# Performance work log

Measured on AMD Instinct MI355X. Metric: run time of the kernel, lower is better.

## Reference

```python
import jax, jax.numpy as jnp
import numpy as np

NUM_EMBEDDINGS = 1024
EMBEDDING_DIM = 256


def setup_inputs() -> dict:
    key = jax.random.key(0)
    k1, k2 = jax.random.split(key)
    x = jax.random.normal(k1, (64, EMBEDDING_DIM, 32, 32), dtype=jnp.float32)
    # torch.nn.init.uniform_ default is U[0,1)
    embeddings = jax.random.uniform(k2, (EMBEDDING_DIM, NUM_EMBEDDINGS), dtype=jnp.float32)
    return {"x": x, "embeddings": embeddings}


def reference(x, embeddings):
    # x: [B, C, H, W] with C == embedding_dim; embeddings: [D, K]
    B, C, H, W = x.shape
    x_perm = jnp.transpose(x, (0, 2, 3, 1))           # [B, H, W, D]
    flat = x_perm.reshape(-1, C)                      # [N, D]
    sim = flat @ embeddings                           # [N, K] GEMM
    dists = (jnp.sum(flat * flat, axis=1, keepdims=True)
             + jnp.sum(embeddings * embeddings, axis=0)
             - 2.0 * sim)                             # [N, K]
    indices = jnp.argmin(dists, axis=1)               # [N]
    # one-hot @ embeddings.T is just a row gather of embeddings.T
    quantized = embeddings.T[indices]                 # [N, D]
    quantized = quantized.reshape(x_perm.shape)       # [B, H, W, D]
    # straight-through estimator
    q_ste = x_perm + jax.lax.stop_gradient(quantized - x_perm)
    q_ste = jnp.transpose(q_ste, (0, 3, 1, 2))        # [B, C, H, W]
    quantized = jnp.transpose(quantized, (0, 3, 1, 2))
    return q_ste, quantized, indices
```

## Files before the change

### kernel.cpp

```cpp
#include <hip/hip_runtime.h>

typedef unsigned short u16;
typedef unsigned int   u32;

#define DCH  256
#define KCB  1024
#define HW   1024
#define NPOS 65536
#define MARGIN 0.12f

#define ESQ_WS   0
#define IDX_WS   4096
#define FCNT_WS  266240
#define FLIST_WS 266304
#define ESQD_WS  528448ull
#define XH_WS    1048576ull
#define EH_WS    34603008ull

using f32x4 = __attribute__((ext_vector_type(4))) float;
using f16x8 = __attribute__((ext_vector_type(8))) _Float16;

__device__ __forceinline__ u16 f2h(float x) {
    _Float16 h = (_Float16)x;
    return *reinterpret_cast<u16*>(&h);
}
__device__ __forceinline__ u32 umin2(u32 a, u32 b) { return a < b ? a : b; }
__device__ __forceinline__ u32 umax2(u32 a, u32 b) { return a > b ? a : b; }

__device__ __forceinline__ void gl_lds16(const void* g, void* l) {
    __builtin_amdgcn_global_load_lds(
        (const __attribute__((address_space(1))) void*)g,
        (__attribute__((address_space(3))) void*)l, 16, 0, 0);
}

__device__ __forceinline__ void transpose_slice(const float* __restrict__ src,
                                                u16* __restrict__ dst,
                                                int b, int pc, int cc, int tid) {
    __shared__ float Xs[32][260];
    const int p0 = pc * 256;
    const int c0 = cc * 32;
    const size_t nbase = (size_t)b * 1024 + p0;
#pragma unroll
    for (int r = 0; r < 8; ++r) {
        int id4 = tid + 256 * r;
        int c = id4 >> 6;
        int q = id4 & 63;
        float4 v = *reinterpret_cast<const float4*>(
            src + (size_t)b * 262144 + (size_t)(c0 + c) * 1024 + p0 + q * 4);
        *reinterpret_cast<float4*>(&Xs[c][q * 4]) = v;
    }
    __syncthreads();
    const int p = tid;
#pragma unroll
    for (int dg = 0; dg < 4; ++dg) {
        u32 w0, w1, w2, w3;
        {
            float f0 = Xs[dg * 8 + 0][p], f1 = Xs[dg * 8 + 1][p];
            float f2 = Xs[dg * 8 + 2][p], f3 = Xs[dg * 8 + 3][p];
            float f4 = Xs[dg * 8 + 4][p], f5 = Xs[dg * 8 + 5][p];
            float f6 = Xs[dg * 8 + 6][p], f7 = Xs[dg * 8 + 7][p];
            w0 = (u32)f2h(f0) | ((u32)f2h(f1) << 16);
            w1 = (u32)f2h(f2) | ((u32)f2h(f3) << 16);
            w2 = (u32)f2h(f4) | ((u32)f2h(f5) << 16);
            w3 = (u32)f2h(f6) | ((u32)f2h(f7) << 16);
        }
        uint4 ov = {w0, w1, w2, w3};
        *reinterpret_cast<uint4*>(dst + (nbase + p) * 256 + c0 + dg * 8) = ov;
    }
}

__global__ __launch_bounds__(256) void prep_all(const float* __restrict__ X,
                                                const float* __restrict__ E,
                                                u16* __restrict__ Xh,
                                                u16* __restrict__ Eh,
                                                float* __restrict__ esq,
                                                double* __restrict__ esqd,
                                                int* __restrict__ fcnt) {
    const int tid = threadIdx.x;
    const int bid = blockIdx.x;
    if (bid < 2048) {
        transpose_slice(X, Xh, bid >> 5, (bid >> 3) & 3, bid & 7, tid);
    } else if (bid < 2080) {
        int b2 = bid - 2048;
        transpose_slice(E, Eh, 0, (b2 >> 3) & 3, b2 & 7, tid);
    } else {
        if (bid == 2080 && tid == 0) *fcnt = 0;
        int k = (bid - 2080) * 256 + tid;
        double s = 0.0;
#pragma unroll 8
        for (int c = 0; c < DCH; ++c) {
            double e = (double)E[c * KCB + k];
            s = fma(e, e, s);
        }
        esq[k] = (float)s;
        esqd[k] = s;
    }
}

#define BUFS  16384
#define EH_O  8192
#define ESQ_O 32768
#define MRG_O 36864
#define SM_SZ 39936

__global__ __launch_bounds__(256, 2) void vq_main_mfma(
        const u16* __restrict__ XhG, const u16* __restrict__ EhG,
        const float* __restrict__ esq,
        int* __restrict__ idx_out, int* __restrict__ flag_cnt,
        int* __restrict__ flag_list) {
    __shared__ alignas(16) char sm[SM_SZ];
    const int tid = threadIdx.x;
    const int l = tid & 63;
    const int w = tid >> 6;
    const int wm = w >> 1, wn = w & 1;
    const int pbase = blockIdx.x * 128;

    *reinterpret_cast<float4*>(sm + ESQ_O + tid * 16) =
        *reinterpret_cast<const float4*>(esq + tid * 4);

    const int rowt0 = w * 32 + (l >> 2);
    const int slog = (l & 3) ^ ((rowt0 >> 1) & 3);
    const char* XhB = reinterpret_cast<const char*>(XhG);
    const char* EhB = reinterpret_cast<const char*>(EhG);
    const size_t xoff0 = (size_t)(pbase + rowt0) * 512 + slog * 16;
    const size_t eoff0 = (size_t)rowt0 * 512 + slog * 16;
    const int w2k = (w * 2) * 1024;

    const int rA = wm * 64 + (l & 15);
    const int addrA = rA * 64 + (((l >> 4) ^ ((rA >> 1) & 3)) * 16);
    const int rB = wn * 64 + (l & 15);
    const int addrB = rB * 64 + (((l >> 4) ^ ((rB >> 1) & 3)) * 16);

    auto STAGE = [&](int bufo, int nt, int dt) {
        size_t xo = xoff0 + (size_t)dt * 64;
        gl_lds16(XhB + xo,        sm + bufo + w2k);
        gl_lds16(XhB + xo + 8192, sm + bufo + w2k + 1024);
        size_t eo = eoff0 + (size_t)nt * 65536 + (size_t)dt * 64;
        gl_lds16(EhB + eo,        sm + bufo + EH_O + w2k);
        gl_lds16(EhB + eo + 8192, sm + bufo + EH_O + w2k + 1024);
    };

    u32 b1[16], b2[16];
#pragma unroll
    for (int q = 0; q < 16; ++q) { b1[q] = 0xFFFFFFFFu; b2[q] = 0xFFFFFFFFu; }

    STAGE(0, 0, 0);
    __syncthreads();

    int step = 0;
    for (int nt = 0; nt < 8; ++nt) {
        f32x4 acc[4][4];
#pragma unroll
        for (int i = 0; i < 4; ++i)
#pragma unroll
            for (int j = 0; j < 4; ++j)
#pragma unroll
                for (int r = 0; r < 4; ++r) acc[i][j][r] = 0.f;

        for (int dt = 0; dt < 8; ++dt) {
            int nxt = step + 1;
            if (nxt < 64) STAGE((nxt & 1) * BUFS, nxt >> 3, nxt & 7);
            const char* bo = sm + (step & 1) * BUFS;
            f16x8 a[4], bh[4];
#pragma unroll
            for (int i = 0; i < 4; ++i)
                a[i] = *reinterpret_cast<const f16x8*>(bo + addrA + i * 1024);
#pragma unroll
            for (int j = 0; j < 4; ++j)
                bh[j] = *reinterpret_cast<const f16x8*>(bo + EH_O + addrB + j * 1024);
#pragma unroll
            for (int i = 0; i < 4; ++i)
#pragma unroll
                for (int j = 0; j < 4; ++j)
                    acc[i][j] = __builtin_amdgcn_mfma_f32_16x16x32_f16(a[i], bh[j], acc[i][j], 0, 0, 0);
            __syncthreads();
            ++step;
        }

        const int kb = nt * 128 + wn * 64 + (l & 15);
        float eq[4];
#pragma unroll
        for (int j = 0; j < 4; ++j)
            eq[j] = *reinterpret_cast<const float*>(sm + ESQ_O + (kb + j * 16) * 4);
#pragma unroll
        for (int i = 0; i < 4; ++i)
#pragma unroll
            for (int j = 0; j < 4; ++j)
#pragma unroll
                for (int r = 0; r < 4; ++r) {
                    float s = fmaxf(fmaf(-2.f, acc[i][j][r], eq[j]), 0.f);
                    u32 v = (__float_as_uint(s) & 0xFFFFFC00u) | (u32)(kb + j * 16);
                    int ri = i * 4 + r;
                    u32 m1 = umin2(b1[ri], v);
                    b2[ri] = umin2(b2[ri], umax2(b1[ri], v));
                    b1[ri] = m1;
                }
    }

#pragma unroll
    for (int m = 1; m <= 8; m <<= 1) {
#pragma unroll
        for (int q = 0; q < 16; ++q) {
            u32 ob1 = (u32)__shfl_xor((int)b1[q], m);
            u32 ob2 = (u32)__shfl_xor((int)b2[q], m);
            u32 mx = umax2(b1[q], ob1);
            b1[q] = umin2(b1[q], ob1);
            b2[q] = umin2(umin2(b2[q], ob2), mx);
        }
    }

    if ((l & 15) == 0) {
#pragma unroll
        for (int i = 0; i < 4; ++i)
#pragma unroll
            for (int r = 0; r < 4; ++r) {
                int q = i * 4 + r;
                int rl = wm * 64 + i * 16 + (l >> 4) * 4 + r;
                *reinterpret_cast<u32*>(sm + MRG_O + (rl * 2 + wn) * 4) = b1[q];
                *reinterpret_cast<u32*>(sm + MRG_O + 1024 + (rl * 2 + wn) * 4) = b2[q];
            }
    }
    __syncthreads();
    if (tid < 128) {
        u32 a1 = *reinterpret_cast<u32*>(sm + MRG_O + (tid * 2 + 0) * 4);
        u32 a2 = *reinterpret_cast<u32*>(sm + MRG_O + 1024 + (tid * 2 + 0) * 4);
        u32 c1 = *reinterpret_cast<u32*>(sm + MRG_O + (tid * 2 + 1) * 4);
        u32 c2 = *reinterpret_cast<u32*>(sm + MRG_O + 1024 + (tid * 2 + 1) * 4);
        u32 P1 = umin2(a1, c1);
        u32 P2 = umin2(umin2(a2, c2), umax2(a1, c1));
        int n = pbase + tid;
        idx_out[n] = (int)(P1 & 1023u);
        float f1 = __uint_as_float(P1 & 0xFFFFFC00u);
        float f2 = __uint_as_float(P2 & 0xFFFFFC00u);
        if (f2 - f1 < MARGIN) {
            int s2 = atomicAdd(flag_cnt, 1);
            flag_list[s2] = n;
        }
    }
}

#define RFPB 4
__global__ __launch_bounds__(256) void vq_repair(const float* __restrict__ X,
                                                 const float* __restrict__ E,
                                                 const double* __restrict__ esqd,
                                                 int* __restrict__ idx_out,
                                                 const int* __restrict__ flag_cnt,
                                                 const int* __restrict__ flag_list) {
    __shared__ double xs[RFPB][256];
    __shared__ double rd[RFPB][256];
    __shared__ int    ri[RFPB][256];
    const int tid = threadIdx.x;
    const int cnt = *flag_cnt;
    for (int f0 = blockIdx.x * RFPB; f0 < cnt; f0 += gridDim.x * RFPB) {
#pragma unroll
        for (int g = 0; g < RFPB; ++g) {
            int f = f0 + g;
            int n = flag_list[f < cnt ? f : f0];
            int b = n >> 10, p = n & 1023;
            xs[g][tid] = (double)X[(size_t)b * 262144 + (size_t)tid * 1024 + p];
        }
        __syncthreads();
        double s[RFPB][4];
#pragma unroll
        for (int g = 0; g < RFPB; ++g)
#pragma unroll
            for (int j = 0; j < 4; ++j) s[g][j] = 0.0;
        const float4* Erow = reinterpret_cast<const float4*>(E) + tid;
#pragma unroll 2
        for (int c = 0; c < 256; ++c) {
            float4 ev = Erow[c * 256];
            double e0 = (double)ev.x, e1 = (double)ev.y, e2 = (double)ev.z, e3 = (double)ev.w;
#pragma unroll
            for (int g = 0; g < RFPB; ++g) {
                double xv = xs[g][c];
                s[g][0] = fma(xv, e0, s[g][0]);
                s[g][1] = fma(xv, e1, s[g][1]);
                s[g][2] = fma(xv, e2, s[g][2]);
                s[g][3] = fma(xv, e3, s[g][3]);
            }
        }
        const int k0 = tid * 4;
        const double eq0 = esqd[k0], eq1 = esqd[k0 + 1], eq2 = esqd[k0 + 2], eq3 = esqd[k0 + 3];
#pragma unroll
        for (int g = 0; g < RFPB; ++g) {
            double d0 = eq0 - 2.0 * s[g][0];
            double d1 = eq1 - 2.0 * s[g][1];
            double d2 = eq2 - 2.0 * s[g][2];
            double d3 = eq3 - 2.0 * s[g][3];
            double bd = d0; int bi = k0;
            if (d1 < bd) { bd = d1; bi = k0 + 1; }
            if (d2 < bd) { bd = d2; bi = k0 + 2; }
            if (d3 < bd) { bd = d3; bi = k0 + 3; }
            rd[g][tid] = bd; ri[g][tid] = bi;
        }
        __syncthreads();
        for (int off = 128; off > 0; off >>= 1) {
            if (tid < off) {
#pragma unroll
                for (int g = 0; g < RFPB; ++g) {
                    double od = rd[g][tid + off]; int oi = ri[g][tid + off];
                    if (od < rd[g][tid] || (od == rd[g][tid] && oi < ri[g][tid])) {
                        rd[g][tid] = od; ri[g][tid] = oi;
                    }
                }
            }
            __syncthreads();
        }
        if (tid < RFPB && (f0 + tid) < cnt) {
            idx_out[flag_list[f0 + tid]] = ri[tid][0];
        }
        __syncthreads();
    }
}

#define WCC 8
__global__ __launch_bounds__(256) void vq_write(const float* __restrict__ E,
                                                const int* __restrict__ idx_ws,
                                                float* __restrict__ out0,
                                                float* __restrict__ out1,
                                                float* __restrict__ out2) {
    __shared__ float Es[WCC][1024];
    const int tid = threadIdx.x;
    const int b   = blockIdx.x >> 5;
    const int cch = blockIdx.x & 31;
#pragma unroll
    for (int r = 0; r < 8; ++r) {
        int id4 = tid + 256 * r;
        int c = id4 >> 8;
        int q = id4 & 255;
        *reinterpret_cast<float4*>(&Es[c][q * 4]) =
            *reinterpret_cast<const float4*>(E + (size_t)(cch * WCC + c) * 1024 + q * 4);
    }
    int4 kv = *reinterpret_cast<const int4*>(idx_ws + b * 1024 + tid * 4);
    __syncthreads();
    if (cch == 0) {
        float4 v = {(float)kv.x, (float)kv.y, (float)kv.z, (float)kv.w};
        *reinterpret_cast<float4*>(out2 + b * 1024 + tid * 4) = v;
    }
#pragma unroll
    for (int c = 0; c < WCC; ++c) {
        float4 v = {Es[c][kv.x], Es[c][kv.y], Es[c][kv.z], Es[c][kv.w]};
        size_t o = (size_t)b * 262144 + (size_t)(cch * WCC + c) * 1024 + tid * 4;
        *reinterpret_cast<float4*>(out0 + o) = v;
        *reinterpret_cast<float4*>(out1 + o) = v;
    }
}

extern "C" void kernel_launch(void* const* d_in, const int* in_sizes, int n_in,
                              void* d_out, int out_size, void* d_ws, size_t ws_size,
                              hipStream_t stream) {
    const float* X = (const float*)d_in[0];
    const float* E = (const float*)d_in[1];
    float* out = (float*)d_out;
    char* ws = (char*)d_ws;

    float* esq   = (float*)(ws + ESQ_WS);
    int* idx     = (int*)(ws + IDX_WS);
    int* fcnt    = (int*)(ws + FCNT_WS);
    int* flist   = (int*)(ws + FLIST_WS);
    double* esqd = (double*)(ws + ESQD_WS);
    u16* Xh      = (u16*)(ws + XH_WS);
    u16* Eh      = (u16*)(ws + EH_WS);

    prep_all<<<2084, 256, 0, stream>>>(X, E, Xh, Eh, esq, esqd, fcnt);
    vq_main_mfma<<<512, 256, 0, stream>>>(Xh, Eh, esq, idx, fcnt, flist);
    vq_repair<<<1024, 256, 0, stream>>>(X, E, esqd, idx, fcnt, flist);
    vq_write<<<2048, 256, 0, stream>>>(E, idx,
                                       out,
                                       out + 16777216,
                                       out + 33554432);
}
```

Baseline: 166.7 us.

## Double K-step per stage with 128-byte swizzled LDS rows, halving barriers

The main MFMA kernel now stages 64 channels (128 bytes per row) per pipeline step instead of 32. A new 8-way XOR swizzle lays out the rows in LDS, and two MFMA sub-steps run per staged tile, so the K loop has 4 iterations instead of 8 and there are half as many __syncthreads per codebook tile. The cost is doubled LDS use (about 71 KB per block), which may limit the two-blocks-per-CU target. The repair kernel also processes 8 flagged positions per block instead of 4.

Measured after the change: 195.5 us. 17.2% more time.

```diff
diff --git a/kernel.cpp b/kernel.cpp
--- a/kernel.cpp
+++ b/kernel.cpp
@@ -97,11 +97,11 @@
     }
 }
 
-#define BUFS  16384
-#define EH_O  8192
-#define ESQ_O 32768
-#define MRG_O 36864
-#define SM_SZ 39936
+#define BUFS  32768
+#define EB_O  16384
+#define ESQ_O 65536
+#define MRG_O 69632
+#define SM_SZ 72704
 
 __global__ __launch_bounds__(256, 2) void vq_main_mfma(
         const u16* __restrict__ XhG, const u16* __restrict__ EhG,
@@ -118,26 +118,25 @@
     *reinterpret_cast<float4*>(sm + ESQ_O + tid * 16) =
         *reinterpret_cast<const float4*>(esq + tid * 4);
 
-    const int rowt0 = w * 32 + (l >> 2);
-    const int slog = (l & 3) ^ ((rowt0 >> 1) & 3);
+    const int srow = w * 32 + (l >> 3);
+    const int sswz = ((l & 7) ^ (l >> 3)) * 16;
     const char* XhB = reinterpret_cast<const char*>(XhG);
     const char* EhB = reinterpret_cast<const char*>(EhG);
-    const size_t xoff0 = (size_t)(pbase + rowt0) * 512 + slog * 16;
-    const size_t eoff0 = (size_t)rowt0 * 512 + slog * 16;
-    const int w2k = (w * 2) * 1024;
-
-    const int rA = wm * 64 + (l & 15);
-    const int addrA = rA * 64 + (((l >> 4) ^ ((rA >> 1) & 3)) * 16);
-    const int rB = wn * 64 + (l & 15);
-    const int addrB = rB * 64 + (((l >> 4) ^ ((rB >> 1) & 3)) * 16);
-
-    auto STAGE = [&](int bufo, int nt, int dt) {
-        size_t xo = xoff0 + (size_t)dt * 64;
-        gl_lds16(XhB + xo,        sm + bufo + w2k);
-        gl_lds16(XhB + xo + 8192, sm + bufo + w2k + 1024);
-        size_t eo = eoff0 + (size_t)nt * 65536 + (size_t)dt * 64;
-        gl_lds16(EhB + eo,        sm + bufo + EH_O + w2k);
-        gl_lds16(EhB + eo + 8192, sm + bufo + EH_O + w2k + 1024);
+    const size_t xbase = (size_t)(pbase + srow) * 512 + sswz;
+    const size_t ebase = (size_t)srow * 512 + sswz;
+
+    const int sA0 = (((l >> 4) ^ (l & 7))) * 16;
+    const int addrA0 = wm * 8192 + (l & 15) * 128 + sA0;
+    const int addrB0 = wn * 8192 + (l & 15) * 128 + sA0;
+
+    auto STAGE = [&](int bufo, int nt, int kt) {
+        const size_t xo = xbase + (size_t)kt * 128;
+        const size_t eo = ebase + (size_t)nt * 65536 + (size_t)kt * 128;
+#pragma unroll
+        for (int k = 0; k < 4; ++k) {
+            gl_lds16(XhB + xo + k * 4096, sm + bufo + (w * 4 + k) * 1024);
+            gl_lds16(EhB + eo + k * 4096, sm + bufo + EB_O + (w * 4 + k) * 1024);
+        }
     };
 
     u32 b1[16], b2[16];
@@ -157,22 +156,26 @@
 #pragma unroll
                 for (int r = 0; r < 4; ++r) acc[i][j][r] = 0.f;
 
-        for (int dt = 0; dt < 8; ++dt) {
+        for (int kt = 0; kt < 4; ++kt) {
             int nxt = step + 1;
-            if (nxt < 64) STAGE((nxt & 1) * BUFS, nxt >> 3, nxt & 7);
+            if (nxt < 32) STAGE((nxt & 1) * BUFS, nxt >> 2, nxt & 3);
             const char* bo = sm + (step & 1) * BUFS;
-            f16x8 a[4], bh[4];
-#pragma unroll
-            for (int i = 0; i < 4; ++i)
-                a[i] = *reinterpret_cast<const f16x8*>(bo + addrA + i * 1024);
-#pragma unroll
-            for (int j = 0; j < 4; ++j)
-                bh[j] = *reinterpret_cast<const f16x8*>(bo + EH_O + addrB + j * 1024);
-#pragma unroll
-            for (int i = 0; i < 4; ++i)
+#pragma unroll
+            for (int ds = 0; ds < 2; ++ds) {
+                const int so = ds * 64;
+                f16x8 a[4], bh[4];
+#pragma unroll
+                for (int i = 0; i < 4; ++i)
+                    a[i] = *reinterpret_cast<const f16x8*>(bo + ((addrA0 ^ so) + i * 2048));
 #pragma unroll
                 for (int j = 0; j < 4; ++j)
-                    acc[i][j] = __builtin_amdgcn_mfma_f32_16x16x32_f16(a[i], bh[j], acc[i][j], 0, 0, 0);
+                    bh[j] = *reinterpret_cast<const f16x8*>(bo + EB_O + ((addrB0 ^ so) + j * 2048));
+#pragma unroll
+                for (int i = 0; i < 4; ++i)
+#pragma unroll
+                    for (int j = 0; j < 4; ++j)
+                        acc[i][j] = __builtin_amdgcn_mfma_f32_16x16x32_f16(a[i], bh[j], acc[i][j], 0, 0, 0);
+            }
             __syncthreads();
             ++step;
         }
@@ -239,7 +242,7 @@
     }
 }
 
-#define RFPB 4
+#define RFPB 8
 __global__ __launch_bounds__(256) void vq_repair(const float* __restrict__ X,
                                                  const float* __restrict__ E,
                                                  const double* __restrict__ esqd,
```
